# Kernel optimization log

Measured on AMD Instinct MI355X. Metric: run time of the kernel, lower is better.

## Reference

```python
import jax, jax.numpy as jnp
import numpy as np

N_HEADS = 16  # cfg.n_heads
ROPE_BASE = 10000.0


def _rope_sin_cos(T, head_dim, dtype):
    # standard NeoX-style rotary tables, shape (T, head_dim)
    inv_freq = 1.0 / (ROPE_BASE ** (jnp.arange(0, head_dim, 2, dtype=jnp.float32) / head_dim))
    freqs = jnp.arange(T, dtype=jnp.float32)[:, None] * inv_freq[None, :]  # (T, hd/2)
    emb = jnp.concatenate([freqs, freqs], axis=-1)                          # (T, hd)
    return jnp.sin(emb).astype(dtype), jnp.cos(emb).astype(dtype)


def _rotate_half(x):
    x1, x2 = jnp.split(x, 2, axis=-1)
    return jnp.concatenate([-x2, x1], axis=-1)


def setup_inputs() -> dict:
    key = jax.random.key(0)
    kx, kq, kp, kl = jax.random.split(key, 4)
    B, T, D = 4, 2048, 2048
    x = jax.random.normal(kx, (B, T, D), dtype=jnp.float32)
    # torch Linear weights: (out_features, in_features), no bias
    Wqkv = jax.random.normal(kq, (3 * D, D), dtype=jnp.float32) * (D ** -0.5)
    Wproj = jax.random.normal(kp, (D, D), dtype=jnp.float32) * (D ** -0.5)
    # padding at the end: valid lengths in [T//2, T]
    lengths = jax.random.randint(kl, (B,), T // 2, T + 1)
    attention_mask = (jnp.arange(T)[None, :] < lengths[:, None]).astype(jnp.int32)
    return {"x": x, "Wqkv": Wqkv, "Wproj": Wproj, "attention_mask": attention_mask}


def reference(x, Wqkv, Wproj, attention_mask):
    B, T, D = x.shape
    H = N_HEADS
    hd = D // H
    qkv = (x @ Wqkv.T).reshape(B, T, 3, H, hd)            # (B,T,3,H,hd)
    q, k, v = (jnp.moveaxis(qkv[:, :, i], 1, 2) for i in range(3))  # each (B,H,T,hd)
    sin, cos = _rope_sin_cos(T, hd, x.dtype)              # (T,hd), broadcast over B,H
    q = q * cos + _rotate_half(q) * sin
    k = k * cos + _rotate_half(k) * sin
    scale = 1.0 / jnp.sqrt(jnp.asarray(hd, x.dtype))
    scores = jnp.einsum("bhqd,bhkd->bhqk", q, k) * scale  # (B,H,T,T)
    causal = jnp.triu(jnp.ones((T, T), dtype=bool), k=1)[None, None]       # (1,1,T,T)
    pad = (attention_mask == 0)[:, None, None, :]                           # (B,1,1,T)
    bias = jnp.where(causal | pad, -jnp.inf, 0.0).astype(x.dtype)
    attn = jax.nn.softmax(scores + bias, axis=-1)
    out = jnp.einsum("bhqk,bhkd->bhqd", attn, v)          # (B,H,T,hd)
    out = jnp.moveaxis(out, 1, 2).reshape(B, T, D)
    return out @ Wproj.T
```

## Files before the change

kernel.cpp:

```cpp
#include <hip/hip_runtime.h>
#include <math.h>

#define B_SZ 4
#define T_SEQ 2048
#define D_MODEL 2048
#define NH 16
#define HD 128

typedef unsigned short u16;
typedef unsigned int u32;
typedef __attribute__((ext_vector_type(8))) short short8;
typedef __attribute__((ext_vector_type(4))) float f32x4;

__device__ __forceinline__ float bf2f(u16 u) {
    return __uint_as_float(((u32)u) << 16);
}
__device__ __forceinline__ u16 f2bf(float f) {
    u32 x = __float_as_uint(f);
    return (u16)((x + 0x7fffu + ((x >> 16) & 1u)) >> 16);
}

__device__ __forceinline__ void gload_lds16(const u16* g, u16* lds) {
    __builtin_amdgcn_global_load_lds(
        (const __attribute__((address_space(1))) u32*)(const void*)g,
        (__attribute__((address_space(3))) u32*)(void*)lds, 16, 0, 0);
}

__global__ __launch_bounds__(256) void cast_kernel(const float* __restrict__ in,
                                                   u16* __restrict__ out, int n4)
{
    int idx = blockIdx.x * 256 + threadIdx.x;
    if (idx < n4) {
        float4 x = ((const float4*)in)[idx];
        ushort4 u;
        u.x = f2bf(x.x); u.y = f2bf(x.y); u.z = f2bf(x.z); u.w = f2bf(x.w);
        ((ushort4*)out)[idx] = u;
    }
}

template <int MODE>
__global__ __launch_bounds__(256) void gemm_bt(
    const u16* __restrict__ A, const u16* __restrict__ W,
    float* __restrict__ C,
    u16* __restrict__ qb, u16* __restrict__ kb, u16* __restrict__ vb,
    int M, int N, int K)
{
    __shared__ u16 As[128 * 32];
    __shared__ u16 Bs[128 * 32];

    const int tid = threadIdx.x;
    const int n0 = blockIdx.x * 128;
    const int m0 = blockIdx.y * 128;
    const int w = tid >> 6, L = tid & 63;
    const int wr = w >> 1, wc = w & 1;

    const int srow = tid >> 2;
    const int sseg = (tid & 3) * 8;
    const u16* Ag = A + (size_t)(m0 + srow) * K + sseg;
    const u16* Wg = W + (size_t)(n0 + srow) * K + sseg;
    u16* AsP = As + tid * 8;
    u16* BsP = Bs + tid * 8;
    const size_t rowK64 = (size_t)64 * K;

    f32x4 acc[4][4];
#pragma unroll
    for (int i = 0; i < 4; ++i)
#pragma unroll
        for (int j = 0; j < 4; ++j) acc[i][j] = (f32x4){0.f, 0.f, 0.f, 0.f};

    const int lr = L & 15;
    const int lq = (L >> 4) * 8;

    for (int k0 = 0; k0 < K; k0 += 32) {
        __syncthreads();
        gload_lds16(Ag + k0, AsP);
        gload_lds16(Ag + k0 + rowK64, AsP + 2048);
        gload_lds16(Wg + k0, BsP);
        gload_lds16(Wg + k0 + rowK64, BsP + 2048);
        __syncthreads();

        short8 a[4], b[4];
#pragma unroll
        for (int i = 0; i < 4; ++i)
            a[i] = *(const short8*)(As + (wr * 64 + i * 16 + lr) * 32 + lq);
#pragma unroll
        for (int j = 0; j < 4; ++j)
            b[j] = *(const short8*)(Bs + (wc * 64 + j * 16 + lr) * 32 + lq);
#pragma unroll
        for (int i = 0; i < 4; ++i)
#pragma unroll
            for (int j = 0; j < 4; ++j)
                acc[i][j] = __builtin_amdgcn_mfma_f32_16x16x32_bf16(
                    a[i], b[j], acc[i][j], 0, 0, 0);
    }

    const int lq4 = (L >> 4) * 4;

    if (MODE == 0) {
#pragma unroll
        for (int i = 0; i < 4; ++i)
#pragma unroll
            for (int j = 0; j < 4; ++j) {
                const int n = n0 + wc * 64 + j * 16 + lr;
#pragma unroll
                for (int r = 0; r < 4; ++r) {
                    const int m = m0 + wr * 64 + i * 16 + lq4 + r;
                    C[(size_t)m * N + n] = acc[i][j][r];
                }
            }
    } else {
        const int s = n0 >> 11;
        const int h = (n0 & 2047) >> 7;
        const int b_ = m0 >> 11;
        const int t0 = m0 & (T_SEQ - 1);
        if (s == 2) {
            __shared__ u16 Cs[128][136];
#pragma unroll
            for (int i = 0; i < 4; ++i)
#pragma unroll
                for (int j = 0; j < 4; ++j)
#pragma unroll
                    for (int r = 0; r < 4; ++r)
                        Cs[wc * 64 + j * 16 + lr][wr * 64 + i * 16 + lq4 + r] =
                            f2bf(acc[i][j][r]);
            __syncthreads();
            u16* vbase = vb + ((size_t)(b_ * NH + h) * HD) * T_SEQ + t0;
#pragma unroll
            for (int it = 0; it < 8; ++it) {
                const int d = it * 16 + (tid >> 4);
                const int tc = (tid & 15) * 8;
                *(short8*)(vbase + (size_t)d * T_SEQ + tc) =
                    *(const short8*)&Cs[d][tc];
            }
        } else {
            u16* p = (s == 0) ? qb : kb;
            u16* pbase = p + ((size_t)(b_ * NH + h) * T_SEQ + t0) * HD;
#pragma unroll
            for (int i = 0; i < 4; ++i)
#pragma unroll
                for (int j = 0; j < 4; ++j) {
                    const int d = wc * 64 + j * 16 + lr;
#pragma unroll
                    for (int r = 0; r < 4; ++r) {
                        const int tl = wr * 64 + i * 16 + lq4 + r;
                        pbase[(size_t)tl * HD + d] = f2bf(acc[i][j][r]);
                    }
                }
        }
    }
}

__global__ __launch_bounds__(128) void rope_kernel(u16* __restrict__ qb,
                                                   u16* __restrict__ kb)
{
    const int bht = blockIdx.x;
    const int t = bht & (T_SEQ - 1);
    const int bh = bht >> 11;
    const int tid = threadIdx.x;
    const int i = tid & 63;
    u16* buf = (tid < 64) ? qb : kb;
    const size_t base = ((size_t)bh * T_SEQ + t) * HD;

    const float inv = expf(-(2.f * (float)i / 128.f) * 9.210340371976184f);
    const float ang = (float)t * inv;
    const float s = sinf(ang);
    const float c = cosf(ang);

    const float x1 = bf2f(buf[base + i]);
    const float x2 = bf2f(buf[base + i + 64]);
    buf[base + i]      = f2bf(x1 * c - x2 * s);
    buf[base + i + 64] = f2bf(x2 * c + x1 * s);
}

__global__ __launch_bounds__(256) void attn_kernel(
    const u16* __restrict__ q, const u16* __restrict__ k,
    const u16* __restrict__ v, const int* __restrict__ mask,
    u16* __restrict__ o)
{
    __shared__ u16 QKs[4 * 64 * 32];
    __shared__ u16 Vt[2 * 128 * 32];
    __shared__ u16 Ps[4][2 * 16 * 32];

    const int tid = threadIdx.x;
    const int id = blockIdx.x;
    const int bh = id & 63;
    const int qi = 31 - (id >> 6);
    const int b = bh >> 4;
    const int q0 = qi * 64;
    const int w = tid >> 6, L = tid & 63;
    const int lr = L & 15;
    const int lq = (L >> 4) * 8;
    const float scale = 0.08838834764831845f;
    const float NEG = -1e30f;

    const u16* qg = q + (size_t)bh * T_SEQ * HD;
    const u16* kg = k + (size_t)bh * T_SEQ * HD;
    const u16* vg = v + (size_t)bh * HD * T_SEQ;
    const int* mrow = mask + b * T_SEQ;

#pragma unroll
    for (int c = 0; c < 4; ++c) {
        const int row = q0 + c * 16 + (L >> 2);
        const int col = w * 32 + (L & 3) * 8;
        gload_lds16(qg + (size_t)row * HD + col,
                    QKs + w * 2048 + c * 512 + L * 8);
    }
    __syncthreads();

    short8 qa[4];
#pragma unroll
    for (int kc = 0; kc < 4; ++kc)
        qa[kc] = *(const short8*)(QKs + kc * 2048 + (w * 16 + lr) * 32 + lq);

    f32x4 on[8];
#pragma unroll
    for (int nd = 0; nd < 8; ++nd) on[nd] = (f32x4){0.f, 0.f, 0.f, 0.f};
    float l_r[4] = {0.f, 0.f, 0.f, 0.f};

    const int row_base = q0 + w * 16 + (L >> 4) * 4;
    u16* PsW = Ps[w];

    for (int kt = 0; kt <= qi; ++kt) {
        const int kv0 = kt * 64;
        __syncthreads();
#pragma unroll
        for (int c = 0; c < 4; ++c) {
            const int row = kv0 + c * 16 + (L >> 2);
            const int col = w * 32 + (L & 3) * 8;
            gload_lds16(kg + (size_t)row * HD + col,
                        QKs + w * 2048 + c * 512 + L * 8);
        }
#pragma unroll
        for (int c = 0; c < 4; ++c) {
            const int kvc = w >> 1;
            const int dg = (w & 1) * 4 + c;
            const int d = dg * 16 + (L >> 2);
            const int t = kv0 + kvc * 32 + (L & 3) * 8;
            gload_lds16(vg + (size_t)d * T_SEQ + t,
                        Vt + kvc * 4096 + dg * 512 + L * 8);
        }
        __syncthreads();

        f32x4 sacc[4];
#pragma unroll
        for (int nt = 0; nt < 4; ++nt) {
            sacc[nt] = (f32x4){0.f, 0.f, 0.f, 0.f};
            short8 bb[4];
#pragma unroll
            for (int kc = 0; kc < 4; ++kc)
                bb[kc] = *(const short8*)(QKs + kc * 2048 + (nt * 16 + lr) * 32 + lq);
#pragma unroll
            for (int kc = 0; kc < 4; ++kc)
                sacc[nt] = __builtin_amdgcn_mfma_f32_16x16x32_bf16(
                    qa[kc], bb[kc], sacc[nt], 0, 0, 0);
        }

        const bool diag = (kt == qi);
        float ps[4][4];
#pragma unroll
        for (int nt = 0; nt < 4; ++nt) {
            const int col = kv0 + nt * 16 + lr;
            const float bias = mrow[col] ? 0.f : NEG;
#pragma unroll
            for (int r = 0; r < 4; ++r) {
                float s = sacc[nt][r] * scale + bias;
                if (diag && col > row_base + r) s = NEG;
                const float p = __expf(s);
                ps[nt][r] = p;
                l_r[r] += p;
            }
        }

#pragma unroll
        for (int nt = 0; nt < 4; ++nt) {
            const int koff = (nt & 1) * 16 + lr;
#pragma unroll
            for (int r = 0; r < 4; ++r)
                PsW[(nt >> 1) * 512 + ((L >> 4) * 4 + r) * 32 + koff] =
                    f2bf(ps[nt][r]);
        }

        short8 pa[2];
#pragma unroll
        for (int kk = 0; kk < 2; ++kk)
            pa[kk] = *(const short8*)(PsW + kk * 512 + lr * 32 + lq);
#pragma unroll
        for (int nd = 0; nd < 8; ++nd) {
            short8 vb0 = *(const short8*)(Vt + 0 * 4096 + (nd * 16 + lr) * 32 + lq);
            short8 vb1 = *(const short8*)(Vt + 1 * 4096 + (nd * 16 + lr) * 32 + lq);
            on[nd] = __builtin_amdgcn_mfma_f32_16x16x32_bf16(pa[0], vb0, on[nd], 0, 0, 0);
            on[nd] = __builtin_amdgcn_mfma_f32_16x16x32_bf16(pa[1], vb1, on[nd], 0, 0, 0);
        }
    }

#pragma unroll
    for (int off = 1; off < 16; off <<= 1)
#pragma unroll
        for (int r = 0; r < 4; ++r)
            l_r[r] += __shfl_xor(l_r[r], off);

    const int h = bh & 15;
#pragma unroll
    for (int r = 0; r < 4; ++r) {
        const float inv = 1.f / l_r[r];
        const int t = row_base + r;
        u16* op = o + ((size_t)(b * T_SEQ + t)) * D_MODEL + h * HD + lr;
#pragma unroll
        for (int nd = 0; nd < 8; ++nd)
            op[nd * 16] = f2bf(on[nd][r] * inv);
    }
}

extern "C" void kernel_launch(void* const* d_in, const int* in_sizes, int n_in,
                              void* d_out, int out_size, void* d_ws, size_t ws_size,
                              hipStream_t stream)
{
    const float* x     = (const float*)d_in[0];
    const float* Wqkv  = (const float*)d_in[1];
    const float* Wproj = (const float*)d_in[2];
    const int*   mask  = (const int*)d_in[3];
    float* out = (float*)d_out;

    const size_t E = (size_t)B_SZ * T_SEQ * D_MODEL;
    u16* xb     = (u16*)d_ws;
    u16* wqkvb  = xb + E;
    u16* wprojb = wqkvb + (size_t)3 * D_MODEL * D_MODEL;
    u16* qb     = wprojb + (size_t)D_MODEL * D_MODEL;
    u16* kb     = qb + E;
    u16* vb     = kb + E;
    u16* ob     = vb + E;

    const int M = B_SZ * T_SEQ;

    cast_kernel<<<dim3((int)(E / 4 / 256)), 256, 0, stream>>>(x, xb, (int)(E / 4));
    cast_kernel<<<dim3(3 * D_MODEL * D_MODEL / 4 / 256), 256, 0, stream>>>(
        Wqkv, wqkvb, 3 * D_MODEL * D_MODEL / 4);
    cast_kernel<<<dim3(D_MODEL * D_MODEL / 4 / 256), 256, 0, stream>>>(
        Wproj, wprojb, D_MODEL * D_MODEL / 4);

    gemm_bt<1><<<dim3(3 * D_MODEL / 128, M / 128), 256, 0, stream>>>(
        xb, wqkvb, nullptr, qb, kb, vb, M, 3 * D_MODEL, D_MODEL);

    rope_kernel<<<dim3(B_SZ * NH * T_SEQ), 128, 0, stream>>>(qb, kb);

    attn_kernel<<<dim3(T_SEQ / 64 * 64), 256, 0, stream>>>(qb, kb, vb, mask, ob);

    gemm_bt<0><<<dim3(D_MODEL / 128, M / 128), 256, 0, stream>>>(
        ob, wprojb, out, nullptr, nullptr, nullptr, M, D_MODEL, D_MODEL);
}
```

Baseline: 676.2 us.

## Replace GEMM with 256x256 tiled, double-buffered, swizzled LDS kernel

Replaces the 128x128 single-stage GEMM with a 256x256 tile, 512-thread kernel that double-buffers 64-wide K slices in 128KB of dynamic LDS. Global-to-LDS loads are interleaved with four MFMA quadrant phases and guarded by explicit waitcnt, barriers and setprio. LDS uses an XOR swizzle to avoid bank conflicts, and blocks are remapped across XCDs. The aim is more data reuse and overlap of memory latency with compute in both projection GEMMs. In exchange it relies on hand-tuned wait counts, uses much more LDS per block and lowers occupancy.

```diff
diff --git a/kernel.cpp b/kernel.cpp
--- a/kernel.cpp
+++ b/kernel.cpp
@@ -38,114 +38,213 @@
     }
 }
 
+#define TSZ 16384
+#define MFMA_B16 __builtin_amdgcn_mfma_f32_16x16x32_bf16
+
 template <int MODE>
-__global__ __launch_bounds__(256) void gemm_bt(
+__global__ __launch_bounds__(512, 2) void gemm256(
     const u16* __restrict__ A, const u16* __restrict__ W,
     float* __restrict__ C,
     u16* __restrict__ qb, u16* __restrict__ kb, u16* __restrict__ vb,
     int M, int N, int K)
 {
-    __shared__ u16 As[128 * 32];
-    __shared__ u16 Bs[128 * 32];
+    extern __shared__ u16 smem[];
 
     const int tid = threadIdx.x;
-    const int n0 = blockIdx.x * 128;
-    const int m0 = blockIdx.y * 128;
+    const int nbx = N >> 8;
+    const int nwg = gridDim.x;
+    const int orig = blockIdx.x;
+    const int wgid = (orig & 7) * (nwg >> 3) + (orig >> 3);
+    const int bx = wgid % nbx, by = wgid / nbx;
+    const int n0 = bx << 8, m0 = by << 8;
+
     const int w = tid >> 6, L = tid & 63;
-    const int wr = w >> 1, wc = w & 1;
-
-    const int srow = tid >> 2;
-    const int sseg = (tid & 3) * 8;
-    const u16* Ag = A + (size_t)(m0 + srow) * K + sseg;
-    const u16* Wg = W + (size_t)(n0 + srow) * K + sseg;
-    u16* AsP = As + tid * 8;
-    u16* BsP = Bs + tid * 8;
-    const size_t rowK64 = (size_t)64 * K;
-
-    f32x4 acc[4][4];
-#pragma unroll
-    for (int i = 0; i < 4; ++i)
+    const int wm = w >> 2, wn = w & 3;
+    const int lr = L & 15;
+    const int lqb = (L >> 4) << 4;
+    const int xorv = (lr & 7) << 4;
+    const int cb0 = lqb ^ xorv;
+    const int cb1 = (64 + lqb) ^ xorv;
+
+    const u16* Ag = A + (size_t)m0 * K;
+    const u16* Wg = W + (size_t)n0 * K;
+
+    const int srow = tid >> 3;
+    const int scb = ((tid << 4) & 127) ^ ((srow & 7) << 4);
+    const size_t goff = (size_t)srow * K + (scb >> 1);
+    const int loff = tid << 3;
+
+    const int NT = K >> 6;
+
+    f32x4 acc[8][4];
+#pragma unroll
+    for (int i = 0; i < 8; ++i)
 #pragma unroll
         for (int j = 0; j < 4; ++j) acc[i][j] = (f32x4){0.f, 0.f, 0.f, 0.f};
 
-    const int lr = L & 15;
-    const int lq = (L >> 4) * 8;
-
-    for (int k0 = 0; k0 < K; k0 += 32) {
-        __syncthreads();
-        gload_lds16(Ag + k0, AsP);
-        gload_lds16(Ag + k0 + rowK64, AsP + 2048);
-        gload_lds16(Wg + k0, BsP);
-        gload_lds16(Wg + k0 + rowK64, BsP + 2048);
-        __syncthreads();
-
-        short8 a[4], b[4];
-#pragma unroll
-        for (int i = 0; i < 4; ++i)
-            a[i] = *(const short8*)(As + (wr * 64 + i * 16 + lr) * 32 + lq);
-#pragma unroll
-        for (int j = 0; j < 4; ++j)
-            b[j] = *(const short8*)(Bs + (wc * 64 + j * 16 + lr) * 32 + lq);
-#pragma unroll
-        for (int i = 0; i < 4; ++i)
-#pragma unroll
-            for (int j = 0; j < 4; ++j)
-                acc[i][j] = __builtin_amdgcn_mfma_f32_16x16x32_bf16(
-                    a[i], b[j], acc[i][j], 0, 0, 0);
-    }
-
-    const int lq4 = (L >> 4) * 4;
+#define ST_A(tt, c) gload_lds16(Ag + (size_t)((c) * 64) * K + (size_t)(tt) * 64 + goff, \
+                                smem + ((tt) & 1) * TSZ + (c) * 4096 + loff)
+#define ST_B(tt, c) gload_lds16(Wg + (size_t)((c) * 64) * K + (size_t)(tt) * 64 + goff, \
+                                smem + 2 * TSZ + ((tt) & 1) * TSZ + (c) * 4096 + loff)
+
+    ST_A(0, 0); ST_A(0, 2); ST_B(0, 0); ST_B(0, 1); ST_B(0, 2); ST_B(0, 3);
+    ST_A(0, 1); ST_A(0, 3);
+    ST_A(1, 0); ST_A(1, 2); ST_B(1, 0); ST_B(1, 1); ST_B(1, 2); ST_B(1, 3);
+    asm volatile("s_waitcnt vmcnt(6)" ::: "memory");
+    __builtin_amdgcn_s_barrier();
+
+    for (int t = 0; t < NT; ++t) {
+        const char* pA = (const char*)(smem + (t & 1) * TSZ) + (wm * 128 + lr) * 128;
+        const char* pB = (const char*)(smem + 2 * TSZ + (t & 1) * TSZ) + (wn * 64 + lr) * 128;
+        short8 alo[4][2], ahi[4][2], blo[2][2], bhi[2][2];
+
+#pragma unroll
+        for (int f = 0; f < 4; ++f) {
+            alo[f][0] = *(const short8*)(pA + f * 2048 + cb0);
+            alo[f][1] = *(const short8*)(pA + f * 2048 + cb1);
+        }
+#pragma unroll
+        for (int g = 0; g < 2; ++g) {
+            blo[g][0] = *(const short8*)(pB + g * 2048 + cb0);
+            blo[g][1] = *(const short8*)(pB + g * 2048 + cb1);
+        }
+        if (t + 1 < NT) { ST_A(t + 1, 1); ST_A(t + 1, 3); }
+        asm volatile("s_waitcnt lgkmcnt(8)" ::: "memory");
+        __builtin_amdgcn_s_barrier();
+        asm volatile("s_waitcnt lgkmcnt(0)" ::: "memory");
+        __builtin_amdgcn_sched_barrier(0);
+        __builtin_amdgcn_s_setprio(1);
+#pragma unroll
+        for (int f = 0; f < 4; ++f)
+#pragma unroll
+            for (int g = 0; g < 2; ++g) {
+                acc[f][g] = MFMA_B16(alo[f][0], blo[g][0], acc[f][g], 0, 0, 0);
+                acc[f][g] = MFMA_B16(alo[f][1], blo[g][1], acc[f][g], 0, 0, 0);
+            }
+        __builtin_amdgcn_s_setprio(0);
+        __builtin_amdgcn_s_barrier();
+
+#pragma unroll
+        for (int g = 0; g < 2; ++g) {
+            bhi[g][0] = *(const short8*)(pB + 4096 + g * 2048 + cb0);
+            bhi[g][1] = *(const short8*)(pB + 4096 + g * 2048 + cb1);
+        }
+        if (t + 2 < NT) { ST_A(t + 2, 0); ST_A(t + 2, 2); }
+        __builtin_amdgcn_s_barrier();
+        asm volatile("s_waitcnt lgkmcnt(0)" ::: "memory");
+        __builtin_amdgcn_sched_barrier(0);
+        __builtin_amdgcn_s_setprio(1);
+#pragma unroll
+        for (int f = 0; f < 4; ++f)
+#pragma unroll
+            for (int g = 0; g < 2; ++g) {
+                acc[f][2 + g] = MFMA_B16(alo[f][0], bhi[g][0], acc[f][2 + g], 0, 0, 0);
+                acc[f][2 + g] = MFMA_B16(alo[f][1], bhi[g][1], acc[f][2 + g], 0, 0, 0);
+            }
+        __builtin_amdgcn_s_setprio(0);
+        __builtin_amdgcn_s_barrier();
+
+#pragma unroll
+        for (int f = 0; f < 4; ++f) {
+            ahi[f][0] = *(const short8*)(pA + 8192 + f * 2048 + cb0);
+            ahi[f][1] = *(const short8*)(pA + 8192 + f * 2048 + cb1);
+        }
+        if (t + 2 < NT) { ST_B(t + 2, 0); ST_B(t + 2, 1); }
+        __builtin_amdgcn_s_barrier();
+        asm volatile("s_waitcnt lgkmcnt(0)" ::: "memory");
+        __builtin_amdgcn_sched_barrier(0);
+        __builtin_amdgcn_s_setprio(1);
+#pragma unroll
+        for (int f = 0; f < 4; ++f)
+#pragma unroll
+            for (int g = 0; g < 2; ++g) {
+                acc[4 + f][g] = MFMA_B16(ahi[f][0], blo[g][0], acc[4 + f][g], 0, 0, 0);
+                acc[4 + f][g] = MFMA_B16(ahi[f][1], blo[g][1], acc[4 + f][g], 0, 0, 0);
+            }
+        __builtin_amdgcn_s_setprio(0);
+        __builtin_amdgcn_s_barrier();
+
+        if (t + 2 < NT) { ST_B(t + 2, 2); ST_B(t + 2, 3); }
+        if (t < NT - 2)
+            asm volatile("s_waitcnt vmcnt(6)" ::: "memory");
+        else
+            asm volatile("s_waitcnt vmcnt(0)" ::: "memory");
+        __builtin_amdgcn_s_barrier();
+        __builtin_amdgcn_s_setprio(1);
+#pragma unroll
+        for (int f = 0; f < 4; ++f)
+#pragma unroll
+            for (int g = 0; g < 2; ++g) {
+                acc[4 + f][2 + g] = MFMA_B16(ahi[f][0], bhi[g][0], acc[4 + f][2 + g], 0, 0, 0);
+                acc[4 + f][2 + g] = MFMA_B16(ahi[f][1], bhi[g][1], acc[4 + f][2 + g], 0, 0, 0);
+            }
+        __builtin_amdgcn_s_setprio(0);
+        __builtin_amdgcn_s_barrier();
+    }
+#undef ST_A
+#undef ST_B
+
+    const int lq4 = (L >> 4) << 2;
 
     if (MODE == 0) {
 #pragma unroll
-        for (int i = 0; i < 4; ++i)
-#pragma unroll
-            for (int j = 0; j < 4; ++j) {
-                const int n = n0 + wc * 64 + j * 16 + lr;
-#pragma unroll
-                for (int r = 0; r < 4; ++r) {
-                    const int m = m0 + wr * 64 + i * 16 + lq4 + r;
-                    C[(size_t)m * N + n] = acc[i][j][r];
-                }
-            }
+        for (int f = 0; f < 8; ++f) {
+            const int m = m0 + wm * 128 + (f >> 2) * 64 + (f & 3) * 16 + lq4;
+#pragma unroll
+            for (int g = 0; g < 4; ++g) {
+                const int n = n0 + wn * 64 + (g >> 1) * 32 + (g & 1) * 16 + lr;
+#pragma unroll
+                for (int r = 0; r < 4; ++r)
+                    C[(size_t)(m + r) * N + n] = acc[f][g][r];
+            }
+        }
     } else {
         const int s = n0 >> 11;
-        const int h = (n0 & 2047) >> 7;
         const int b_ = m0 >> 11;
         const int t0 = m0 & (T_SEQ - 1);
         if (s == 2) {
-            __shared__ u16 Cs[128][136];
-#pragma unroll
-            for (int i = 0; i < 4; ++i)
-#pragma unroll
-                for (int j = 0; j < 4; ++j)
+            u16* Ts = smem;
+#pragma unroll
+            for (int f = 0; f < 8; ++f) {
+                const int tl = wm * 128 + (f >> 2) * 64 + (f & 3) * 16 + lq4;
+#pragma unroll
+                for (int g = 0; g < 4; ++g) {
+                    const int c = wn * 64 + (g >> 1) * 32 + (g & 1) * 16 + lr;
+                    char* rowp = (char*)Ts + c * 512;
 #pragma unroll
                     for (int r = 0; r < 4; ++r)
-                        Cs[wc * 64 + j * 16 + lr][wr * 64 + i * 16 + lq4 + r] =
-                            f2bf(acc[i][j][r]);
+                        *(u16*)(rowp + (((tl + r) * 2) ^ ((c & 7) << 4))) =
+                            f2bf(acc[f][g][r]);
+                }
+            }
             __syncthreads();
-            u16* vbase = vb + ((size_t)(b_ * NH + h) * HD) * T_SEQ + t0;
-#pragma unroll
-            for (int it = 0; it < 8; ++it) {
-                const int d = it * 16 + (tid >> 4);
-                const int tc = (tid & 15) * 8;
-                *(short8*)(vbase + (size_t)d * T_SEQ + tc) =
-                    *(const short8*)&Cs[d][tc];
+            const int h0 = (n0 & 2047) >> 7;
+            const int tcb = (tid & 31) << 4;
+#pragma unroll
+            for (int pass = 0; pass < 16; ++pass) {
+                const int c = pass * 16 + (tid >> 5);
+                short8 vv = *(const short8*)((const char*)Ts + c * 512 +
+                                             (tcb ^ ((c & 7) << 4)));
+                const int hh = c >> 7, d = c & 127;
+                *(short8*)(vb + ((size_t)(b_ * NH + h0 + hh) * HD + d) * T_SEQ +
+                           t0 + (tcb >> 1)) = vv;
             }
         } else {
             u16* p = (s == 0) ? qb : kb;
-            u16* pbase = p + ((size_t)(b_ * NH + h) * T_SEQ + t0) * HD;
-#pragma unroll
-            for (int i = 0; i < 4; ++i)
-#pragma unroll
-                for (int j = 0; j < 4; ++j) {
-                    const int d = wc * 64 + j * 16 + lr;
-#pragma unroll
-                    for (int r = 0; r < 4; ++r) {
-                        const int tl = wr * 64 + i * 16 + lq4 + r;
-                        pbase[(size_t)tl * HD + d] = f2bf(acc[i][j][r]);
-                    }
+            const int nb = n0 & 2047;
+#pragma unroll
+            for (int f = 0; f < 8; ++f) {
+                const int tl = t0 + wm * 128 + (f >> 2) * 64 + (f & 3) * 16 + lq4;
+#pragma unroll
+                for (int g = 0; g < 4; ++g) {
+                    const int nn = nb + wn * 64 + (g >> 1) * 32 + (g & 1) * 16 + lr;
+                    const int hh = nn >> 7, d = nn & 127;
+                    u16* pb = p + ((size_t)(b_ * NH + hh) * T_SEQ + tl) * HD + d;
+#pragma unroll
+                    for (int r = 0; r < 4; ++r)
+                        pb[(size_t)r * HD] = f2bf(acc[f][g][r]);
                 }
+            }
         }
     }
 }
@@ -338,13 +437,13 @@
     cast_kernel<<<dim3(D_MODEL * D_MODEL / 4 / 256), 256, 0, stream>>>(
         Wproj, wprojb, D_MODEL * D_MODEL / 4);
 
-    gemm_bt<1><<<dim3(3 * D_MODEL / 128, M / 128), 256, 0, stream>>>(
+    gemm256<1><<<dim3((3 * D_MODEL / 256) * (M / 256)), 512, 131072, stream>>>(
         xb, wqkvb, nullptr, qb, kb, vb, M, 3 * D_MODEL, D_MODEL);
 
     rope_kernel<<<dim3(B_SZ * NH * T_SEQ), 128, 0, stream>>>(qb, kb);
 
     attn_kernel<<<dim3(T_SEQ / 64 * 64), 256, 0, stream>>>(qb, kb, vb, mask, ob);
 
-    gemm_bt<0><<<dim3(D_MODEL / 128, M / 128), 256, 0, stream>>>(
+    gemm256<0><<<dim3((D_MODEL / 256) * (M / 256)), 512, 131072, stream>>>(
         ob, wprojb, out, nullptr, nullptr, nullptr, M, D_MODEL, D_MODEL);
 }
```

Result: faster. 577.6 us (-14.6%).
